# Kernel optimization log

Measured on AMD Instinct MI355X. Metric: run time of the kernel, lower is better.

## Reference

```python
import jax, jax.numpy as jnp
import numpy as np

NUM_GROUPS = 4
EPS = 1e-6


def group_norm(x, scale, bias):
    # x: (b, c, f, h, w), normalize per group over (c//G, f, h, w) in fp32
    b, c, f, h, w = x.shape
    xg = x.astype(jnp.float32).reshape(b, NUM_GROUPS, c // NUM_GROUPS, f, h, w)
    mean = xg.mean(axis=(2, 3, 4, 5), keepdims=True)
    var = xg.var(axis=(2, 3, 4, 5), keepdims=True)
    xn = ((xg - mean) * jax.lax.rsqrt(var + EPS)).reshape(b, c, f, h, w)
    return (xn * scale[None, :, None, None, None] + bias[None, :, None, None, None]).astype(x.dtype)


def conv1x1x1(x, w, b):
    # 1x1x1 Conv3d == channel-mixing linear. w: (c_out, c_in), b: (c_out,)
    return jnp.einsum('bcfhw,oc->bofhw', x, w) + b[None, :, None, None, None]


def setup_inputs() -> dict:
    key = jax.random.key(0)
    ks = jax.random.split(key, 9)
    c = 256
    x = jax.random.normal(ks[0], (6, c, 48, 48), dtype=jnp.float32)  # (3*b, c, h, w), b=2
    init = lambda k: (jax.random.normal(k, (c, c), dtype=jnp.float32) * 0.02)
    return {
        'x': x,
        'gn_scale': jnp.ones((c,), jnp.float32),
        'gn_bias': jnp.zeros((c,), jnp.float32),
        'wq': init(ks[1]), 'bq': jnp.zeros((c,), jnp.float32),
        'wk': init(ks[2]), 'bk': jnp.zeros((c,), jnp.float32),
        'wv': init(ks[3]), 'bv': jnp.zeros((c,), jnp.float32),
        'wp': init(ks[4]), 'bp': jnp.zeros((c,), jnp.float32),
    }


def reference(x, gn_scale, gn_bias, wq, bq, wk, bk, wv, bv, wp, bp):
    b3, c, hh, ww = x.shape
    b = b3 // 3
    # chunk(x, 3) along batch, stack at dim 2 -> (b, c, f=3, h, w)
    h_ = x.reshape(3, b, c, hh, ww).transpose(1, 2, 0, 3, 4)
    h_ = group_norm(h_, gn_scale, gn_bias)
    q = conv1x1x1(h_, wq, bq)
    k = conv1x1x1(h_, wk, bk)
    v = conv1x1x1(h_, wv, bv)
    f = 3
    n = f * hh * ww
    qf = q.reshape(b, c, n).transpose(0, 2, 1)  # (b, n, c)
    kf = k.reshape(b, c, n)                     # (b, c, n)
    vf = v.reshape(b, c, n)                     # (b, c, n)
    scale = jnp.float32(c) ** -0.5
    scores = jnp.einsum('bic,bcj->bij', qf.astype(jnp.float32), kf.astype(jnp.float32)) * scale
    attn = jax.nn.softmax(scores, axis=2).astype(x.dtype)  # (b, n, n)
    # bmm(v, attn^T): out[b,c,i] = sum_j v[b,c,j] * attn[b,i,j]
    h_ = jnp.einsum('bcj,bij->bci', vf, attn).reshape(b, c, f, hh, ww)
    h_ = conv1x1x1(h_, wp, bp)
    # (b, c, f, h, w) -> (b, f, c, h, w) -> (b*f, c, h, w)
    h_ = h_.transpose(0, 2, 1, 3, 4).reshape(b * f, c, hh, ww)
    return x + h_
```

## Files before the change

kernel.cpp:

```cpp
#include <hip/hip_runtime.h>
#include <hip/hip_bf16.h>

#define NPOS 6912
#define HW   2304
#define C    256
#define EPSG 1e-6f
#define K2 (0.0625f * 1.4426950408889634f)

typedef __attribute__((ext_vector_type(8))) short bf16x8;
typedef __attribute__((ext_vector_type(4))) float f32x4;
typedef long long i64;
typedef unsigned char u8;

__device__ __forceinline__ unsigned short f2bf(float f) {
    union { float f; unsigned int u; } v; v.f = f;
    unsigned int lsb = (v.u >> 16) & 1u;
    return (unsigned short)((v.u + 0x7fffu + lsb) >> 16);
}

__device__ __forceinline__ u8 f2fp8(float f) {
    union { float f; unsigned u; } v; v.f = f;
    unsigned sgn = (v.u >> 24) & 0x80u;
    unsigned a = v.u & 0x7FFFFFFFu;
    if (a >= 0x3C800000u) {
        unsigned r = a + 0x000FFFFFu + ((a >> 20) & 1u);
        return (u8)(sgn | ((r >> 20) - 0x3C0u));
    }
    union { unsigned u; float f; } w2; w2.u = a;
    int mnt = (int)rintf(w2.f * 512.0f);
    return (u8)(sgn | (unsigned)mnt);
}

__device__ __forceinline__ float fp8tof(u8 v) {
    unsigned u = ((unsigned)(v & 0x80u) << 24) | ((((unsigned)(v & 0x7Fu)) + 960u) << 20);
    union { unsigned u; float f; } w; w.u = u;
    return w.f;
}

#define MFMA(a, b, c)  __builtin_amdgcn_mfma_f32_16x16x32_bf16((a), (b), (c), 0, 0, 0)
#define MFMA8(a, b, c) __builtin_amdgcn_mfma_f32_16x16x32_fp8_fp8((a), (b), (c), 0, 0, 0)

__device__ __forceinline__ void gld16(const u8* g, const char* l) {
    __builtin_amdgcn_global_load_lds(
        (const __attribute__((address_space(1))) void*)(unsigned long long)g,
        (__attribute__((address_space(3))) void*)(unsigned int)(unsigned long long)l,
        16, 0, 0);
}


__global__ __launch_bounds__(256) void gn_stats(const float* x, float* part,
                                                const float* wq, const float* wk,
                                                const float* wv, const float* wp,
                                                unsigned short* wbf) {
    if (blockIdx.x < 256) {
        int i = blockIdx.x * 256 + threadIdx.x;
        int o = i >> 8, c = i & 255;
        int pos = (((o >> 6) * 4 + ((o >> 4) & 3)) * 8 + (c >> 5)) * 512
                + (((c >> 3) & 3) * 16 + (o & 15)) * 8 + (c & 7);
        wbf[pos]          = f2bf(wq[i]);
        wbf[65536 + pos]  = f2bf(wk[i]);
        wbf[131072 + pos] = f2bf(wv[i]);
        wbf[196608 + pos] = f2bf(wp[i]);
    }
    int gid = blockIdx.x / 108, slice = blockIdx.x % 108;
    int b = gid >> 2, grp = gid & 3;
    float s = 0.f, s2 = 0.f;
    #pragma unroll
    for (int k = 0; k < 16; ++k) {
        int e = slice * 4096 + k * 256 + (int)threadIdx.x;
        int f = e / 147456; int r1 = e - f * 147456;
        int ch = r1 / HW;   int sp = r1 - ch * HW;
        float v = x[(size_t)((f * 2 + b) * C + grp * 64 + ch) * HW + sp];
        s += v; s2 += v * v;
    }
    #pragma unroll
    for (int off = 32; off; off >>= 1) { s += __shfl_xor(s, off); s2 += __shfl_xor(s2, off); }
    __shared__ float ls[8];
    int w = threadIdx.x >> 6;
    if ((threadIdx.x & 63) == 0) { ls[w * 2] = s; ls[w * 2 + 1] = s2; }
    __syncthreads();
    if (threadIdx.x == 0) {
        float t = 0.f, t2 = 0.f;
        for (int i2 = 0; i2 < 4; ++i2) { t += ls[i2 * 2]; t2 += ls[i2 * 2 + 1]; }
        part[blockIdx.x * 2] = t; part[blockIdx.x * 2 + 1] = t2;
    }
}

__global__ __launch_bounds__(256) void gn_apply(const float* x, const float* part,
                                                const float* gsc, const float* gbi,
                                                unsigned short* hnf) {
    int blk = blockIdx.x;
    int b = blk / 144; int f = (blk % 144) / 48; int y = blk % 48;
    int c = threadIdx.x;
    int gid = b * 4 + (c >> 6);
    float s = 0.f, s2 = 0.f;
    for (int i = 0; i < 108; ++i) {
        s  += part[(gid * 108 + i) * 2];
        s2 += part[(gid * 108 + i) * 2 + 1];
    }
    float mean = s / 442368.f;
    float rsig = rsqrtf(s2 / 442368.f - mean * mean + EPSG);
    float sc = gsc[c] * rsig, bi = gbi[c] - mean * sc;
    __shared__ unsigned short lds[48 * 256];
    const float* xr = x + (size_t)((f * 2 + b) * C + c) * HW + y * 48;
    #pragma unroll
    for (int xw = 0; xw < 48; xw += 4) {
        float4 v = *(const float4*)(xr + xw);
        lds[(xw + 0) * 256 + c] = f2bf(v.x * sc + bi);
        lds[(xw + 1) * 256 + c] = f2bf(v.y * sc + bi);
        lds[(xw + 2) * 256 + c] = f2bf(v.z * sc + bi);
        lds[(xw + 3) * 256 + c] = f2bf(v.w * sc + bi);
    }
    __syncthreads();
    int kc = c >> 5, gg = (c >> 3) & 3, j = c & 7;
    int nbase = f * HW + y * 48;
    for (int xw = 0; xw < 48; ++xw) {
        int n = nbase + xw;
        size_t idx = ((size_t)(((b * 108 + (n >> 6)) * 4 + ((n >> 4) & 3)) * 8 + kc)) * 512
                   + (gg * 16 + (n & 15)) * 8 + j;
        hnf[idx] = lds[xw * 256 + c];
    }
}

__global__ __launch_bounds__(256) void qkv_gemm(const unsigned short* hnf, const unsigned short* wbf,
                                                const float* bq, const float* bk, const float* bvp,
                                                u8* qfp, u8* kfp, u8* vfp) {
    __shared__ u8 tr[4096];
    int t = blockIdx.x;
    int tid = (int)threadIdx.x;
    int lane = tid & 63, w = tid >> 6;
    int l16 = lane & 15, g = lane >> 4;
    f32x4 acc[4] = {{0.f,0.f,0.f,0.f},{0.f,0.f,0.f,0.f},{0.f,0.f,0.f,0.f},{0.f,0.f,0.f,0.f}};
    if (t < 1728) {
        int sel = t / 864; int rem = t % 864;
        int b = rem / 432;  int rem2 = rem % 432;
        int pt = rem2 >> 2; int ot = rem2 & 3;
        const unsigned short* wsel = wbf + sel * 65536;
        const float* bias = sel ? bk : bq;
        u8* out = sel ? kfp : qfp;
        const unsigned short* af  = hnf + (size_t)(((b * 108 + pt) * 4 + w) * 8) * 512 + lane * 8;
        const unsigned short* bfm = wsel + (size_t)(ot * 4 * 8) * 512 + lane * 8;
        #pragma unroll
        for (int kk = 0; kk < 8; ++kk) {
            bf16x8 a = *(const bf16x8*)(af + kk * 512);
            #pragma unroll
            for (int f = 0; f < 4; ++f) {
                bf16x8 bb = *(const bf16x8*)(bfm + (f * 8 + kk) * 512);
                acc[f] = MFMA(a, bb, acc[f]);
            }
        }
        #pragma unroll
        for (int f = 0; f < 4; ++f) {
            int cb = f * 16 + l16;
            int kkl = cb >> 5, gg = (cb >> 3) & 3, by = cb & 7;
            float bv = bias[ot * 64 + cb];
            #pragma unroll
            for (int r = 0; r < 4; ++r)
                tr[((w * 2 + kkl) * 64 + gg * 16 + 4 * g + r) * 8 + by] = f2fp8(acc[f][r] + bv);
        }
        __syncthreads();
        size_t frag = (size_t)((b * 108 + pt) * 4 + (tid >> 6)) * 8 + ot * 2 + ((tid >> 5) & 1);
        *(int4*)(out + frag * 512 + (tid & 31) * 16) = *(const int4*)(tr + tid * 16);
    } else {
        int tv = t - 1728;
        int b = tv / 432; int rem2 = tv % 432;
        int ot = rem2 / 108; int pt = rem2 % 108;
        const unsigned short* wvw = wbf + 131072;
        const unsigned short* afm = wvw + (size_t)((ot * 4 + w) * 8) * 512 + lane * 8;
        const unsigned short* bfm = hnf + (size_t)((b * 108 + pt) * 4 * 8) * 512 + lane * 8;
        #pragma unroll
        for (int kk = 0; kk < 8; ++kk) {
            bf16x8 a = *(const bf16x8*)(afm + kk * 512);
            #pragma unroll
            for (int f = 0; f < 4; ++f) {
                bf16x8 bb = *(const bf16x8*)(bfm + (f * 8 + kk) * 512);
                acc[f] = MFMA(a, bb, acc[f]);
            }
        }
        #pragma unroll
        for (int f = 0; f < 4; ++f) {
            int nb = f * 16 + l16;
            int kk2 = nb >> 5, gg = (nb >> 3) & 3, j = nb & 7;
            #pragma unroll
            for (int r = 0; r < 4; ++r) {
                int o = ot * 64 + w * 16 + 4 * g + r;
                tr[((w * 2 + kk2) * 64 + gg * 16 + 4 * g + r) * 8 + j] = f2fp8(acc[f][r] + bvp[o]);
            }
        }
        __syncthreads();
        size_t frag = (size_t)((b * 108 + pt) * 16 + ot * 4 + (tid >> 6)) * 2 + ((tid >> 5) & 1);
        *(int4*)(vfp + frag * 512 + (tid & 31) * 16) = *(const int4*)(tr + tid * 16);
    }
}

__global__ __launch_bounds__(512, 2) void flash(const u8* qf, const u8* kf, const u8* vf,
                                                u8* po, float* lsg) {
    __shared__ char smem[65536];
    int blk = blockIdx.x;
    int x = blk & 7, qt = blk >> 3;
    int b = x >> 2, ks = x & 3;
    int slot = ks * 2 + b;
    int tid = (int)threadIdx.x;
    int lane = tid & 63, w = tid >> 6;
    int l16 = lane & 15, g = lane >> 4;
    int i0 = qt * 256 + w * 32;

    i64 qa[2][8];
    #pragma unroll
    for (int u = 0; u < 2; ++u) {
        const u8* qb = qf + (size_t)((((size_t)b * 108 + qt * 4 + (w >> 1)) * 4
                                      + (w & 1) * 2 + u) * 8) * 512 + lane * 8;
        #pragma unroll
        for (int kk = 0; kk < 8; ++kk)
            qa[u][kk] = *(const i64*)(qb + kk * 512);
    }

    int srcA = (g & 1) * 32 + l16;
    int srcB = srcA + 16;
    int gh = g >> 1;

    size_t tb = (size_t)(b * 108 + ks * 27) * 16384;
    const u8* kst[2]; const u8* vst[2];
    #pragma unroll
    for (int q = 0; q < 2; ++q) {
        kst[q] = kf + tb + (q * 8 + w) * 1024 + lane * 16;
        vst[q] = vf + tb + (q * 8 + w) * 1024 + lane * 16;
    }
    #pragma unroll
    for (int q = 0; q < 2; ++q) {
        gld16(kst[q], smem + (q * 8 + w) * 1024);
        gld16(vst[q], smem + 16384 + (q * 8 + w) * 1024);
        kst[q] += 16384; vst[q] += 16384;
    }

    f32x4 oacc[2][16];
    #pragma unroll
    for (int u = 0; u < 2; ++u)
        #pragma unroll
        for (int cf = 0; cf < 16; ++cf) oacc[u][cf] = (f32x4){0.f,0.f,0.f,0.f};
    f32x4 oaccL[2];
    oaccL[0] = (f32x4){0.f,0.f,0.f,0.f};
    oaccL[1] = (f32x4){0.f,0.f,0.f,0.f};
    const i64 ONES = 0x3838383838383838LL;

    __syncthreads();

    for (int it = 0; it < 27; ++it) {
        int cur = it & 1;
        if (it < 26) {
            int db = (cur ^ 1) * 32768;
            #pragma unroll
            for (int q = 0; q < 2; ++q) {
                gld16(kst[q], smem + db + (q * 8 + w) * 1024);
                gld16(vst[q], smem + db + 16384 + (q * 8 + w) * 1024);
                kst[q] += 16384; vst[q] += 16384;
            }
        }
        int kb = cur * 32768;
        int vb = kb + 16384;

        f32x4 s4[2][4];
        #pragma unroll
        for (int u = 0; u < 2; ++u)
            #pragma unroll
            for (int f = 0; f < 4; ++f) s4[u][f] = (f32x4){0.f,0.f,0.f,0.f};
        const char* kp = smem + kb + lane * 8;
        __builtin_amdgcn_s_setprio(1);
        #pragma unroll
        for (int kk = 0; kk < 8; ++kk) {
            #pragma unroll
            for (int f = 0; f < 4; ++f) {
                i64 kv = *(const i64*)(kp + (f * 8 + kk) * 512);
                s4[0][f] = MFMA8(kv, qa[0][kk], s4[0][f]);
                s4[1][f] = MFMA8(kv, qa[1][kk], s4[1][f]);
            }
        }
        __builtin_amdgcn_s_setprio(0);

        int d_[2][4];
        #pragma unroll
        for (int u = 0; u < 2; ++u)
            #pragma unroll
            for (int f = 0; f < 4; ++f) {
                float p0 = __builtin_amdgcn_exp2f(fminf(s4[u][f][0] * K2, 8.f));
                float p1 = __builtin_amdgcn_exp2f(fminf(s4[u][f][1] * K2, 8.f));
                float p2 = __builtin_amdgcn_exp2f(fminf(s4[u][f][2] * K2, 8.f));
                float p3 = __builtin_amdgcn_exp2f(fminf(s4[u][f][3] * K2, 8.f));
                int lo = __builtin_amdgcn_cvt_pk_fp8_f32(p0, p1, 0, false);
                d_[u][f] = __builtin_amdgcn_cvt_pk_fp8_f32(p2, p3, lo, true);
            }

        const char* vp = smem + vb + lane * 8;
        #pragma unroll
        for (int kk2 = 0; kk2 < 2; ++kk2) {
            i64 pa[2];
            #pragma unroll
            for (int u = 0; u < 2; ++u) {
                int lo0 = __shfl(d_[u][2 * kk2],     srcA);
                int lo1 = __shfl(d_[u][2 * kk2 + 1], srcA);
                int hi0 = __shfl(d_[u][2 * kk2],     srcB);
                int hi1 = __shfl(d_[u][2 * kk2 + 1], srcB);
                unsigned int plo = (unsigned int)(gh ? lo1 : lo0);
                unsigned int phi = (unsigned int)(gh ? hi1 : hi0);
                pa[u] = (i64)plo | ((i64)phi << 32);
            }
            __builtin_amdgcn_s_setprio(1);
            oaccL[0] = MFMA8(pa[0], ONES, oaccL[0]);
            oaccL[1] = MFMA8(pa[1], ONES, oaccL[1]);
            #pragma unroll
            for (int cf = 0; cf < 16; ++cf) {
                i64 vv8 = *(const i64*)(vp + (cf * 2 + kk2) * 512);
                oacc[0][cf] = MFMA8(pa[0], vv8, oacc[0][cf]);
                oacc[1][cf] = MFMA8(pa[1], vv8, oacc[1][cf]);
            }
            __builtin_amdgcn_s_setprio(0);
        }
        __syncthreads();
    }

    #pragma unroll
    for (int u = 0; u < 2; ++u) {
        size_t pb = ((size_t)slot * NPOS + i0 + u * 16) * C;
        #pragma unroll
        for (int cf = 0; cf < 16; ++cf)
            #pragma unroll
            for (int r = 0; r < 4; ++r)
                po[pb + (size_t)(4 * g + r) * C + cf * 16 + l16] = f2fp8(oacc[u][cf][r]);
        if (l16 == 0) {
            #pragma unroll
            for (int r = 0; r < 4; ++r)
                lsg[(size_t)slot * NPOS + i0 + u * 16 + 4 * g + r] = oaccL[u][r];
        }
    }
}

__global__ __launch_bounds__(256) void proj(const u8* po, const float* lsg,
                                            const unsigned short* wbf,
                                            const float* bp, const float* x, float* out) {
    int t = blockIdx.x;
    int b = t / 432; int rem2 = t % 432;
    int pt = rem2 >> 2; int ot = rem2 & 3;
    int lane = threadIdx.x & 63, w = threadIdx.x >> 6;
    int l16 = lane & 15, g = lane >> 4;
    int n = pt * 64 + w * 16 + l16;
    float l = 0.f;
    #pragma unroll
    for (int ks2 = 0; ks2 < 4; ++ks2) l += lsg[(size_t)(ks2 * 2 + b) * NPOS + n];
    float rl = 1.f / l;
    const unsigned short* wpw = wbf + 196608;
    const unsigned short* bfm = wpw + (size_t)(ot * 4 * 8) * 512 + lane * 8;
    const u8* prow = po + ((size_t)b * NPOS + n) * C + g * 8;
    f32x4 acc[4] = {{0.f,0.f,0.f,0.f},{0.f,0.f,0.f,0.f},{0.f,0.f,0.f,0.f},{0.f,0.f,0.f,0.f}};
    #pragma unroll
    for (int kk = 0; kk < 8; ++kk) {
        float av0 = 0.f, av1 = 0.f, av2 = 0.f, av3 = 0.f;
        float av4 = 0.f, av5 = 0.f, av6 = 0.f, av7 = 0.f;
        #pragma unroll
        for (int ks2 = 0; ks2 < 4; ++ks2) {
            i64 p8 = *(const i64*)(prow + (size_t)ks2 * (2 * NPOS * 256) + kk * 32);
            av0 += fp8tof((u8)(p8));        av1 += fp8tof((u8)(p8 >> 8));
            av2 += fp8tof((u8)(p8 >> 16));  av3 += fp8tof((u8)(p8 >> 24));
            av4 += fp8tof((u8)(p8 >> 32));  av5 += fp8tof((u8)(p8 >> 40));
            av6 += fp8tof((u8)(p8 >> 48));  av7 += fp8tof((u8)(p8 >> 56));
        }
        bf16x8 a;
        a[0] = (short)f2bf(av0 * rl); a[1] = (short)f2bf(av1 * rl);
        a[2] = (short)f2bf(av2 * rl); a[3] = (short)f2bf(av3 * rl);
        a[4] = (short)f2bf(av4 * rl); a[5] = (short)f2bf(av5 * rl);
        a[6] = (short)f2bf(av6 * rl); a[7] = (short)f2bf(av7 * rl);
        #pragma unroll
        for (int f = 0; f < 4; ++f) {
            bf16x8 bb = *(const bf16x8*)(bfm + (f * 8 + kk) * 512);
            acc[f] = MFMA(a, bb, acc[f]);
        }
    }
    __shared__ float lt[64][72];
    #pragma unroll
    for (int f = 0; f < 4; ++f) {
        float bv = bp[ot * 64 + f * 16 + l16];
        #pragma unroll
        for (int r = 0; r < 4; ++r)
            lt[f * 16 + l16][w * 16 + 4 * g + r] = acc[f][r] + bv;
    }
    __syncthreads();
    int p0 = pt * 64;
    int f3 = p0 / HW; int sp0 = p0 - f3 * HW;
    for (int it = 0; it < 16; ++it) {
        int ol = it * 4 + w;
        int pl = lane;
        size_t idx = ((size_t)(b * 3 + f3) * C + ot * 64 + ol) * HW + sp0 + pl;
        out[idx] = x[idx] + lt[ol][pl];
    }
}

extern "C" void kernel_launch(void* const* d_in, const int* in_sizes, int n_in,
                              void* d_out, int out_size, void* d_ws, size_t ws_size,
                              hipStream_t stream) {
    const float* x   = (const float*)d_in[0];
    const float* gsc = (const float*)d_in[1];
    const float* gbi = (const float*)d_in[2];
    const float* wq  = (const float*)d_in[3];
    const float* bq  = (const float*)d_in[4];
    const float* wk  = (const float*)d_in[5];
    const float* bk  = (const float*)d_in[6];
    const float* wv  = (const float*)d_in[7];
    const float* bv  = (const float*)d_in[8];
    const float* wp  = (const float*)d_in[9];
    const float* bp  = (const float*)d_in[10];

    char* ws = (char*)d_ws;
    unsigned short* wbf = (unsigned short*)(ws);
    float* part         = (float*)(ws + 524288);
    unsigned short* hn  = (unsigned short*)(ws + 532480);
    u8* qfp             = (u8*)(ws + 7610368);
    u8* kfp             = (u8*)(ws + 11149312);
    u8* vfp             = (u8*)(ws + 14688256);
    u8* po              = (u8*)(ws + 18227200);
    float* lsg          = (float*)(ws + 32382976);
    float* out = (float*)d_out;

    hipLaunchKernelGGL(gn_stats, dim3(864),  dim3(256), 0, stream, x, part, wq, wk, wv, wp, wbf);
    hipLaunchKernelGGL(gn_apply, dim3(288),  dim3(256), 0, stream, x, part, gsc, gbi, hn);
    hipLaunchKernelGGL(qkv_gemm, dim3(2592), dim3(256), 0, stream, hn, wbf, bq, bk, bv, qfp, kfp, vfp);
    hipLaunchKernelGGL(flash,    dim3(216),  dim3(512), 0, stream, qfp, kfp, vfp, po, lsg);
    hipLaunchKernelGGL(proj,     dim3(864),  dim3(256), 0, stream, po, lsg, wbf, bp, x, out);
}
```

Before: 155.1 us.

## Switch flash attention to wide-K scaled FP8 MFMA with LDS-staged P tiles

Replaces the 16x16x32 FP8 MFMAs in the flash kernel with the larger MX-scaled 16x16x128 (QK^T) and 32x32x64 (PV) f8f6f4 instructions, using unit scales. The Q/K/V producers rewrite their fragment layouts to match the new operand shapes. Probabilities are staged through an extra LDS region instead of being rearranged with lane shuffles. The row sum is now computed with VALU adds and shuffle-xor instead of an extra MFMA against a ones vector. This aims to cut MFMA instruction count and shuffle overhead, but raises LDS use to 80KB, which may limit occupancy at two blocks per CU, and adds LDS round trips for P.

```diff
diff --git a/kernel.cpp b/kernel.cpp
--- a/kernel.cpp
+++ b/kernel.cpp
@@ -9,6 +9,8 @@
 
 typedef __attribute__((ext_vector_type(8))) short bf16x8;
 typedef __attribute__((ext_vector_type(4))) float f32x4;
+typedef __attribute__((ext_vector_type(16))) float f32x16;
+typedef __attribute__((ext_vector_type(8))) int v8i;
 typedef long long i64;
 typedef unsigned char u8;
 
@@ -38,7 +40,15 @@
 }
 
 #define MFMA(a, b, c)  __builtin_amdgcn_mfma_f32_16x16x32_bf16((a), (b), (c), 0, 0, 0)
-#define MFMA8(a, b, c) __builtin_amdgcn_mfma_f32_16x16x32_fp8_fp8((a), (b), (c), 0, 0, 0)
+#define MFMAS16(a, b, c) __builtin_amdgcn_mfma_scale_f32_16x16x128_f8f6f4((a), (b), (c), 0, 0, 0, 0x7F7F7F7F, 0, 0x7F7F7F7F)
+#define MFMAS32(a, b, c) __builtin_amdgcn_mfma_scale_f32_32x32x64_f8f6f4((a), (b), (c), 0, 0, 0, 0x7F7F7F7F, 0, 0x7F7F7F7F)
+
+__device__ __forceinline__ v8i mk8(int4 lo, int4 hi) {
+    v8i r;
+    r[0] = lo.x; r[1] = lo.y; r[2] = lo.z; r[3] = lo.w;
+    r[4] = hi.x; r[5] = hi.y; r[6] = hi.z; r[7] = hi.w;
+    return r;
+}
 
 __device__ __forceinline__ void gld16(const u8* g, const char* l) {
     __builtin_amdgcn_global_load_lds(
@@ -151,16 +161,17 @@
         }
         #pragma unroll
         for (int f = 0; f < 4; ++f) {
-            int cb = f * 16 + l16;
-            int kkl = cb >> 5, gg = (cb >> 3) & 3, by = cb & 7;
-            float bv = bias[ot * 64 + cb];
+            float bv = bias[ot * 64 + f * 16 + l16];
             #pragma unroll
             for (int r = 0; r < 4; ++r)
-                tr[((w * 2 + kkl) * 64 + gg * 16 + 4 * g + r) * 8 + by] = f2fp8(acc[f][r] + bv);
+                tr[w * 1024 + (f & 1) * 512 + ((f >> 1) * 16 + 4 * g + r) * 16 + l16]
+                    = f2fp8(acc[f][r] + bv);
         }
         __syncthreads();
-        size_t frag = (size_t)((b * 108 + pt) * 4 + (tid >> 6)) * 8 + ot * 2 + ((tid >> 5) & 1);
-        *(int4*)(out + frag * 512 + (tid & 31) * 16) = *(const int4*)(tr + tid * 16);
+        int t2 = tid >> 6, hf = (tid >> 5) & 1, ln = tid & 31;
+        size_t frag = ((size_t)(b * 108 + pt) * 4 + t2) * 2 + (ot >> 1);
+        *(int4*)(out + frag * 2048 + hf * 1024 + ((ot & 1) * 32 + ln) * 16)
+            = *(const int4*)(tr + tid * 16);
     } else {
         int tv = t - 1728;
         int b = tv / 432; int rem2 = tv % 432;
@@ -179,23 +190,23 @@
         }
         #pragma unroll
         for (int f = 0; f < 4; ++f) {
-            int nb = f * 16 + l16;
-            int kk2 = nb >> 5, gg = (nb >> 3) & 3, j = nb & 7;
             #pragma unroll
             for (int r = 0; r < 4; ++r) {
                 int o = ot * 64 + w * 16 + 4 * g + r;
-                tr[((w * 2 + kk2) * 64 + gg * 16 + 4 * g + r) * 8 + j] = f2fp8(acc[f][r] + bvp[o]);
+                tr[(w >> 1) * 2048 + (f & 1) * 1024
+                   + ((f >> 1) * 32 + (w & 1) * 16 + 4 * g + r) * 16 + l16]
+                    = f2fp8(acc[f][r] + bvp[o]);
             }
         }
         __syncthreads();
-        size_t frag = (size_t)((b * 108 + pt) * 16 + ot * 4 + (tid >> 6)) * 2 + ((tid >> 5) & 1);
-        *(int4*)(vfp + frag * 512 + (tid & 31) * 16) = *(const int4*)(tr + tid * 16);
+        size_t frag = (size_t)(b * 108 + pt) * 8 + ot * 2 + (tid >> 7);
+        *(int4*)(vfp + frag * 2048 + (tid & 127) * 16) = *(const int4*)(tr + tid * 16);
     }
 }
 
 __global__ __launch_bounds__(512, 2) void flash(const u8* qf, const u8* kf, const u8* vf,
                                                 u8* po, float* lsg) {
-    __shared__ char smem[65536];
+    __shared__ char smem[81920];
     int blk = blockIdx.x;
     int x = blk & 7, qt = blk >> 3;
     int b = x >> 2, ks = x & 3;
@@ -205,19 +216,15 @@
     int l16 = lane & 15, g = lane >> 4;
     int i0 = qt * 256 + w * 32;
 
-    i64 qa[2][8];
-    #pragma unroll
-    for (int u = 0; u < 2; ++u) {
-        const u8* qb = qf + (size_t)((((size_t)b * 108 + qt * 4 + (w >> 1)) * 4
-                                      + (w & 1) * 2 + u) * 8) * 512 + lane * 8;
-        #pragma unroll
-        for (int kk = 0; kk < 8; ++kk)
-            qa[u][kk] = *(const i64*)(qb + kk * 512);
-    }
-
-    int srcA = (g & 1) * 32 + l16;
-    int srcB = srcA + 16;
-    int gh = g >> 1;
+    v8i qa[2][2];
+    #pragma unroll
+    for (int u = 0; u < 2; ++u)
+        #pragma unroll
+        for (int h = 0; h < 2; ++h) {
+            const u8* qb = qf + ((((size_t)b * 108 + qt * 4 + (w >> 1)) * 4
+                                  + ((2 * w + u) & 3)) * 2 + h) * 2048 + lane * 16;
+            qa[u][h] = mk8(*(const int4*)qb, *(const int4*)(qb + 1024));
+        }
 
     size_t tb = (size_t)(b * 108 + ks * 27) * 16384;
     const u8* kst[2]; const u8* vst[2];
@@ -233,15 +240,13 @@
         kst[q] += 16384; vst[q] += 16384;
     }
 
-    f32x4 oacc[2][16];
-    #pragma unroll
-    for (int u = 0; u < 2; ++u)
-        #pragma unroll
-        for (int cf = 0; cf < 16; ++cf) oacc[u][cf] = (f32x4){0.f,0.f,0.f,0.f};
-    f32x4 oaccL[2];
-    oaccL[0] = (f32x4){0.f,0.f,0.f,0.f};
-    oaccL[1] = (f32x4){0.f,0.f,0.f,0.f};
-    const i64 ONES = 0x3838383838383838LL;
+    f32x16 oacc[8];
+    #pragma unroll
+    for (int ct = 0; ct < 8; ++ct)
+        #pragma unroll
+        for (int r = 0; r < 16; ++r) oacc[ct][r] = 0.f;
+    float lsum0 = 0.f, lsum1 = 0.f;
+    int pbase = 65536 + w * 2048;
 
     __syncthreads();
 
@@ -263,55 +268,50 @@
         #pragma unroll
         for (int u = 0; u < 2; ++u)
             #pragma unroll
-            for (int f = 0; f < 4; ++f) s4[u][f] = (f32x4){0.f,0.f,0.f,0.f};
-        const char* kp = smem + kb + lane * 8;
+            for (int tt = 0; tt < 4; ++tt) s4[u][tt] = (f32x4){0.f,0.f,0.f,0.f};
         __builtin_amdgcn_s_setprio(1);
         #pragma unroll
-        for (int kk = 0; kk < 8; ++kk) {
-            #pragma unroll
-            for (int f = 0; f < 4; ++f) {
-                i64 kv = *(const i64*)(kp + (f * 8 + kk) * 512);
-                s4[0][f] = MFMA8(kv, qa[0][kk], s4[0][f]);
-                s4[1][f] = MFMA8(kv, qa[1][kk], s4[1][f]);
+        for (int tt = 0; tt < 4; ++tt) {
+            #pragma unroll
+            for (int h = 0; h < 2; ++h) {
+                const char* ka = smem + kb + (tt * 2 + h) * 2048 + lane * 16;
+                v8i a = mk8(*(const int4*)ka, *(const int4*)(ka + 1024));
+                s4[0][tt] = MFMAS16(a, qa[0][h], s4[0][tt]);
+                s4[1][tt] = MFMAS16(a, qa[1][h], s4[1][tt]);
             }
         }
         __builtin_amdgcn_s_setprio(0);
 
-        int d_[2][4];
-        #pragma unroll
-        for (int u = 0; u < 2; ++u)
-            #pragma unroll
-            for (int f = 0; f < 4; ++f) {
-                float p0 = __builtin_amdgcn_exp2f(fminf(s4[u][f][0] * K2, 8.f));
-                float p1 = __builtin_amdgcn_exp2f(fminf(s4[u][f][1] * K2, 8.f));
-                float p2 = __builtin_amdgcn_exp2f(fminf(s4[u][f][2] * K2, 8.f));
-                float p3 = __builtin_amdgcn_exp2f(fminf(s4[u][f][3] * K2, 8.f));
+        #pragma unroll
+        for (int u = 0; u < 2; ++u) {
+            float rs = 0.f;
+            #pragma unroll
+            for (int tt = 0; tt < 4; ++tt) {
+                float p0 = __builtin_amdgcn_exp2f(fminf(s4[u][tt][0] * K2, 8.f));
+                float p1 = __builtin_amdgcn_exp2f(fminf(s4[u][tt][1] * K2, 8.f));
+                float p2 = __builtin_amdgcn_exp2f(fminf(s4[u][tt][2] * K2, 8.f));
+                float p3 = __builtin_amdgcn_exp2f(fminf(s4[u][tt][3] * K2, 8.f));
+                rs += (p0 + p1) + (p2 + p3);
                 int lo = __builtin_amdgcn_cvt_pk_fp8_f32(p0, p1, 0, false);
-                d_[u][f] = __builtin_amdgcn_cvt_pk_fp8_f32(p2, p3, lo, true);
-            }
-
-        const char* vp = smem + vb + lane * 8;
-        #pragma unroll
-        for (int kk2 = 0; kk2 < 2; ++kk2) {
-            i64 pa[2];
-            #pragma unroll
-            for (int u = 0; u < 2; ++u) {
-                int lo0 = __shfl(d_[u][2 * kk2],     srcA);
-                int lo1 = __shfl(d_[u][2 * kk2 + 1], srcA);
-                int hi0 = __shfl(d_[u][2 * kk2],     srcB);
-                int hi1 = __shfl(d_[u][2 * kk2 + 1], srcB);
-                unsigned int plo = (unsigned int)(gh ? lo1 : lo0);
-                unsigned int phi = (unsigned int)(gh ? hi1 : hi0);
-                pa[u] = (i64)plo | ((i64)phi << 32);
-            }
+                int d  = __builtin_amdgcn_cvt_pk_fp8_f32(p2, p3, lo, true);
+                *(int*)(smem + pbase + u * 1024 + (tt >> 1) * 512 + l16 * 32
+                        + (tt & 1) * 16 + g * 4) = d;
+            }
+            rs += __shfl_xor(rs, 16);
+            rs += __shfl_xor(rs, 32);
+            if (u == 0) lsum0 += rs; else lsum1 += rs;
+        }
+
+        {
+            const char* pp = smem + pbase + ((lane >> 4) & 1) * 1024 + (lane >> 5) * 512
+                           + l16 * 32;
+            v8i pa = mk8(*(const int4*)pp, *(const int4*)(pp + 16));
             __builtin_amdgcn_s_setprio(1);
-            oaccL[0] = MFMA8(pa[0], ONES, oaccL[0]);
-            oaccL[1] = MFMA8(pa[1], ONES, oaccL[1]);
-            #pragma unroll
-            for (int cf = 0; cf < 16; ++cf) {
-                i64 vv8 = *(const i64*)(vp + (cf * 2 + kk2) * 512);
-                oacc[0][cf] = MFMA8(pa[0], vv8, oacc[0][cf]);
-                oacc[1][cf] = MFMA8(pa[1], vv8, oacc[1][cf]);
+            #pragma unroll
+            for (int ct = 0; ct < 8; ++ct) {
+                const char* va = smem + vb + ct * 2048 + lane * 16;
+                v8i vv = mk8(*(const int4*)va, *(const int4*)(va + 1024));
+                oacc[ct] = MFMAS32(pa, vv, oacc[ct]);
             }
             __builtin_amdgcn_s_setprio(0);
         }
@@ -319,18 +319,15 @@
     }
 
     #pragma unroll
-    for (int u = 0; u < 2; ++u) {
-        size_t pb = ((size_t)slot * NPOS + i0 + u * 16) * C;
-        #pragma unroll
-        for (int cf = 0; cf < 16; ++cf)
-            #pragma unroll
-            for (int r = 0; r < 4; ++r)
-                po[pb + (size_t)(4 * g + r) * C + cf * 16 + l16] = f2fp8(oacc[u][cf][r]);
-        if (l16 == 0) {
-            #pragma unroll
-            for (int r = 0; r < 4; ++r)
-                lsg[(size_t)slot * NPOS + i0 + u * 16 + 4 * g + r] = oaccL[u][r];
-        }
+    for (int ct = 0; ct < 8; ++ct)
+        #pragma unroll
+        for (int r = 0; r < 16; ++r) {
+            int n = i0 + (r & 3) + 8 * (r >> 2) + 4 * (lane >> 5);
+            po[((size_t)slot * NPOS + n) * C + ct * 32 + (lane & 31)] = f2fp8(oacc[ct][r]);
+        }
+    if (lane < 16) {
+        lsg[(size_t)slot * NPOS + i0 + lane]      = lsum0;
+        lsg[(size_t)slot * NPOS + i0 + 16 + lane] = lsum1;
     }
 }
 
```

Result: faster. 141.6 us (-8.7%).
